# Performance work log

Measured on AMD Instinct MI355X. Metric: run time of the kernel, lower is better.

## Reference

```python
import jax, jax.numpy as jnp
import numpy as np

N_QUBITS = 4
N_LAYERS = 2
DIM = 1 << N_QUBITS  # 16-dim state vector

# --- fixed (parameter-free) CNOT entangler layers, precomputed as 16x16 permutations ---

def _cnot_perm(c, t):
    M = np.zeros((DIM, DIM), np.complex64)
    for b in range(DIM):
        b2 = b ^ (1 << (N_QUBITS - 1 - t)) if (b >> (N_QUBITS - 1 - c)) & 1 else b
        M[b2, b] = 1.0
    return M

def _entangler(r):
    E = np.eye(DIM, dtype=np.complex64)
    for i in range(N_QUBITS):  # pennylane applies CNOT(i, (i+r)%n) sequentially
        E = _cnot_perm(i, (i + r) % N_QUBITS) @ E
    return E

ENT = [jnp.asarray(_entangler((l % (N_QUBITS - 1)) + 1)) for l in range(N_LAYERS)]
# Z_TABLE[b, w] = <b| Z_w |b>
Z_TABLE = jnp.asarray(np.array([[1.0 - 2.0 * ((b >> (N_QUBITS - 1 - w)) & 1) for w in range(N_QUBITS)] for b in range(DIM)], np.float32))


def _rot(phi, theta, omega):
    # pennylane Rot = RZ(omega) @ RY(theta) @ RZ(phi)
    c = jnp.cos(theta / 2).astype(jnp.complex64)
    s = jnp.sin(theta / 2).astype(jnp.complex64)
    a = jnp.exp(-0.5j * (phi + omega)) * c
    b = -jnp.exp(0.5j * (phi - omega)) * s
    cc = jnp.exp(-0.5j * (phi - omega)) * s
    d = jnp.exp(0.5j * (phi + omega)) * c
    return jnp.stack([jnp.stack([a, b]), jnp.stack([cc, d])])


def _vqc_unitary(weights):
    # weights: [N_LAYERS, N_QUBITS, 3] -> 16x16 unitary for StronglyEntanglingLayers
    U = jnp.eye(DIM, dtype=jnp.complex64)
    for l in range(N_LAYERS):
        R = _rot(weights[l, 0, 0], weights[l, 0, 1], weights[l, 0, 2])
        for q in range(1, N_QUBITS):  # wire 0 is most-significant bit -> left kron factor
            R = jnp.kron(R, _rot(weights[l, q, 0], weights[l, q, 1], weights[l, q, 2]))
        U = ENT[l] @ (R @ U)
    return U


def _vqc(x, weights):
    # x: [..., 4] rotation angles; AngleEmbedding uses RX: RX(a)|0> = [cos(a/2), -i sin(a/2)]
    c = jnp.cos(x / 2).astype(jnp.complex64)
    s = jnp.sin(x / 2).astype(jnp.complex64)
    amp = jnp.stack([c, -1j * s], axis=-1)  # [..., 4, 2]
    psi0 = jnp.einsum('...a,...b,...c,...d->...abcd', amp[..., 0, :], amp[..., 1, :], amp[..., 2, :], amp[..., 3, :])
    psi0 = psi0.reshape(x.shape[:-1] + (DIM,))
    U = _vqc_unitary(weights)
    psi = jnp.einsum('ij,...j->...i', U, psi0)
    probs = psi.real ** 2 + psi.imag ** 2
    return probs @ Z_TABLE  # [..., 4] PauliZ expectation values


def setup_inputs() -> dict:
    key = jax.random.key(0)
    k0, k1, k2, k3 = jax.random.split(key, 4)
    H = 768
    B, S = 8, 2048
    embeddings = jax.random.normal(k0, (B, S, H), dtype=jnp.float32)
    lim = 1.0 / np.sqrt(H)
    Wq = jax.random.normal(k1, (N_QUBITS, H), dtype=jnp.float32) * lim
    Wk = jax.random.normal(k2, (N_QUBITS, H), dtype=jnp.float32) * lim
    bq = jnp.zeros((N_QUBITS,), jnp.float32)
    bk = jnp.zeros((N_QUBITS,), jnp.float32)
    vqc_weights = jax.random.uniform(k3, (N_LAYERS, N_QUBITS, 3), dtype=jnp.float32) * (2.0 * np.pi)
    return {'embeddings': embeddings, 'Wq': Wq, 'bq': bq, 'Wk': Wk, 'bk': bk, 'vqc_weights': vqc_weights}


def reference(embeddings, Wq, bq, Wk, bk, vqc_weights):
    Q = jnp.einsum('bsh,qh->bsq', embeddings, Wq) + bq  # [B,S,4]
    K = jnp.einsum('bsh,qh->bsq', embeddings, Wk) + bk
    Qv = _vqc(Q, vqc_weights)  # [B,S,4]
    Kv = _vqc(K, vqc_weights)
    attn = jax.nn.softmax(jnp.einsum('bsq,btq->bst', Qv, Kv), axis=-1)  # [B,S,S]
    return jnp.einsum('bst,bth->bsh', attn, embeddings)
```

## Files before the change

kernel.cpp:

```cpp
#include <hip/hip_runtime.h>

#define NB 8
#define NS 2048
#define NH 768
#define NPOS (NB*NS)

typedef short short8 __attribute__((ext_vector_type(8)));
typedef float floatx4 __attribute__((ext_vector_type(4)));

__device__ __forceinline__ unsigned pack_bf16(unsigned b0, unsigned b1) {
  return __builtin_amdgcn_perm(b1, b0, 0x07060302u);
}

#define GLOAD_LDS16(gp, lp) __builtin_amdgcn_global_load_lds( \
  (const __attribute__((address_space(1))) unsigned int*)(gp), \
  (__attribute__((address_space(3))) unsigned int*)(lp), 16, 0, 0)

__global__ __launch_bounds__(384) void epre_kernel(
    const float* __restrict__ E, const float* __restrict__ wts,
    float* __restrict__ Vre, float* __restrict__ Vim,
    unsigned short* __restrict__ ET) {
  int tc = blockIdx.x, hb = blockIdx.y, b = blockIdx.z;
  int tid = threadIdx.x;

  if (tc == 0 && hb == 0 && b == 0 && tid < 16) {
    int j = tid;
    float ar[16], ai[16];
#pragma unroll
    for (int i = 0; i < 16; i++) { ar[i] = (i == j) ? 1.f : 0.f; ai[i] = 0.f; }
#pragma unroll
    for (int l = 0; l < 2; l++) {
#pragma unroll
      for (int q = 0; q < 4; q++) {
        float phi = wts[(l*4+q)*3+0];
        float th  = wts[(l*4+q)*3+1];
        float om  = wts[(l*4+q)*3+2];
        float ct = cosf(0.5f*th), st = sinf(0.5f*th);
        float sm = 0.5f*(phi+om), df = 0.5f*(phi-om);
        float cs = cosf(sm), ss = sinf(sm), cd = cosf(df), sd = sinf(df);
        float Ar =  cs*ct, Ai = -ss*ct;
        float Br = -cd*st, Bi = -sd*st;
        float Cr =  cd*st, Ci = -sd*st;
        float Dr =  cs*ct, Di =  ss*ct;
        int pb = 1 << (3-q);
#pragma unroll
        for (int b0 = 0; b0 < 16; b0++) {
          if (b0 & pb) continue;
          int b1 = b0 | pb;
          float xr = ar[b0], xi = ai[b0], yr = ar[b1], yi = ai[b1];
          ar[b0] = Ar*xr - Ai*xi + Br*yr - Bi*yi;
          ai[b0] = Ar*xi + Ai*xr + Br*yi + Bi*yr;
          ar[b1] = Cr*xr - Ci*xi + Dr*yr - Di*yi;
          ai[b1] = Cr*xi + Ci*xr + Dr*yi + Di*yr;
        }
      }
      const int r = (l == 0) ? 1 : 2;
#pragma unroll
      for (int i2 = 0; i2 < 4; i2++) {
        int cb = 1 << (3-i2);
        int tb = 1 << (3-((i2+r)&3));
#pragma unroll
        for (int b0 = 0; b0 < 16; b0++) {
          if ((b0 & cb) && !(b0 & tb)) {
            int b1 = b0 | tb;
            float tr = ar[b0], ti = ai[b0];
            ar[b0] = ar[b1]; ai[b0] = ai[b1];
            ar[b1] = tr;     ai[b1] = ti;
          }
        }
      }
    }
    int pc = __popc((unsigned)j) & 3;
#pragma unroll
    for (int i = 0; i < 16; i++) {
      float vr = ar[i], vi = ai[i], orr, oi;
      if      (pc == 0) { orr =  vr; oi =  vi; }
      else if (pc == 1) { orr =  vi; oi = -vr; }
      else if (pc == 2) { orr = -vr; oi = -vi; }
      else              { orr = -vi; oi =  vr; }
      Vre[i*16+j] = orr;
      Vim[i*16+j] = oi;
    }
  }

  size_t tbase = ((size_t)((b*4 + hb)*64 + tc)) * 12288;
  const float* Eb = E + (size_t)b*NS*NH + (size_t)tc*32*NH + hb*192;
#pragma unroll
  for (int u = 0; u < 2; u++) {
    int unit = tid + 384*u;
    int q2 = unit / 192, h2 = unit % 192;
    unsigned hi4[4], lo4[4];
#pragma unroll
    for (int jp = 0; jp < 4; jp++) {
      float ea = Eb[(size_t)(q2*8 + 2*jp    )*NH + h2];
      float eb = Eb[(size_t)(q2*8 + 2*jp + 1)*NH + h2];
      unsigned ba = __float_as_uint(ea), bb = __float_as_uint(eb);
      float la = ea - __uint_as_float(ba & 0xFFFF0000u);
      float lb = eb - __uint_as_float(bb & 0xFFFF0000u);
      hi4[jp] = pack_bf16(ba, bb);
      lo4[jp] = pack_bf16(__float_as_uint(la), __float_as_uint(lb));
    }
    int off = h2*32 + ((q2 ^ ((h2>>1)&3))*8);
    *(uint4*)&ET[tbase + off]        = make_uint4(hi4[0],hi4[1],hi4[2],hi4[3]);
    *(uint4*)&ET[tbase + 6144 + off] = make_uint4(lo4[0],lo4[1],lo4[2],lo4[3]);
  }
}

__global__ __launch_bounds__(256) void proj_vqc_kernel(
    const float* __restrict__ E, const float* __restrict__ Wq, const float* __restrict__ bq,
    const float* __restrict__ Wk, const float* __restrict__ bk,
    const float* __restrict__ Vre, const float* __restrict__ Vim,
    float* __restrict__ Qv, float* __restrict__ Kv) {
  __shared__ __align__(16) float WqL[768*4];
  __shared__ __align__(16) float WkL[768*4];
  __shared__ float Vsh[2][16*17];
  int tid = threadIdx.x;
  for (int idx = tid; idx < 768*4; idx += 256) {
    int e = idx >> 2, w = idx & 3;
    WqL[e*4+w] = Wq[w*768+e];
    WkL[e*4+w] = Wk[w*768+e];
  }
  if (tid < 256) {
    int i = tid >> 4, jj = tid & 15;
    Vsh[0][i*17+jj] = Vre[tid];
    Vsh[1][i*17+jj] = Vim[tid];
  }
  __syncthreads();
  float bqr0=bq[0], bqr1=bq[1], bqr2=bq[2], bqr3=bq[3];
  float bkr0=bk[0], bkr1=bk[1], bkr2=bk[2], bkr3=bk[3];
  int lane = tid & 63;
  int wid  = blockIdx.x*4 + (tid >> 6);
  int nw   = gridDim.x*4;
  int grp  = lane >> 4;
  int i    = lane & 15;
  for (int pos = wid; pos < NPOS; pos += nw) {
    const float* er = E + (size_t)pos*768;
    float pq[4] = {0.f,0.f,0.f,0.f};
    float pk[4] = {0.f,0.f,0.f,0.f};
#pragma unroll
    for (int k2 = 0; k2 < 3; k2++) {
      float4 ev = *(const float4*)(er + lane*4 + 256*k2);
#pragma unroll
      for (int jj = 0; jj < 4; jj++) {
        int e = lane*4 + 256*k2 + jj;
        float evs = (jj==0) ? ev.x : (jj==1) ? ev.y : (jj==2) ? ev.z : ev.w;
        float4 wq4 = *(const float4*)&WqL[e*4];
        float4 wk4 = *(const float4*)&WkL[e*4];
        pq[0] += evs*wq4.x; pq[1] += evs*wq4.y; pq[2] += evs*wq4.z; pq[3] += evs*wq4.w;
        pk[0] += evs*wk4.x; pk[1] += evs*wk4.y; pk[2] += evs*wk4.z; pk[3] += evs*wk4.w;
      }
    }
    float part[8];
#pragma unroll
    for (int w = 0; w < 8; w++) {
      float v = (w < 4) ? pq[w] : pk[w-4];
      v += __shfl_xor(v, 32); v += __shfl_xor(v, 16); v += __shfl_xor(v, 8);
      v += __shfl_xor(v, 4);  v += __shfl_xor(v, 2);  v += __shfl_xor(v, 1);
      part[w] = v;
    }
    if (grp < 2) {
      float a0,a1,a2,a3;
      if (grp == 0) { a0=part[0]+bqr0; a1=part[1]+bqr1; a2=part[2]+bqr2; a3=part[3]+bqr3; }
      else          { a0=part[4]+bkr0; a1=part[5]+bkr1; a2=part[6]+bkr2; a3=part[7]+bkr3; }
      float c0=cosf(0.5f*a0), s0=sinf(0.5f*a0);
      float c1=cosf(0.5f*a1), s1=sinf(0.5f*a1);
      float c2=cosf(0.5f*a2), s2=sinf(0.5f*a2);
      float c3=cosf(0.5f*a3), s3=sinf(0.5f*a3);
      float m[16];
#pragma unroll
      for (int j2 = 0; j2 < 16; j2++) {
        float f0 = (j2 & 8) ? s0 : c0;
        float f1 = (j2 & 4) ? s1 : c1;
        float f2 = (j2 & 2) ? s2 : c2;
        float f3 = (j2 & 1) ? s3 : c3;
        m[j2] = f0*f1*f2*f3;
      }
      float re = 0.f, im = 0.f;
#pragma unroll
      for (int j2 = 0; j2 < 16; j2++) {
        re += Vsh[0][i*17+j2]*m[j2];
        im += Vsh[1][i*17+j2]*m[j2];
      }
      float pr = re*re + im*im;
      float r0 = (i & 8) ? -pr : pr;
      float r1 = (i & 4) ? -pr : pr;
      float r2 = (i & 2) ? -pr : pr;
      float r3 = (i & 1) ? -pr : pr;
#pragma unroll
      for (int off = 8; off >= 1; off >>= 1) {
        r0 += __shfl_xor(r0, off);
        r1 += __shfl_xor(r1, off);
        r2 += __shfl_xor(r2, off);
        r3 += __shfl_xor(r3, off);
      }
      if (i == 0) {
        float* dst = (grp == 0 ? Qv : Kv) + (size_t)pos*4;
        dst[0]=r0; dst[1]=r1; dst[2]=r2; dst[3]=r3;
      }
    }
  }
}

#define TKC 32

__global__ __launch_bounds__(512, 4) void attn_kernel(
    const unsigned short* __restrict__ ET, const float* __restrict__ Qv,
    const float* __restrict__ Kv, float* __restrict__ out) {
  int sblk = blockIdx.x;
  int hblk = blockIdx.y;
  int b    = blockIdx.z;
  int tid  = threadIdx.x;
  int lane = tid & 63;
  int w    = tid >> 6;

  __shared__ __align__(16) unsigned short sA[8192];
  __shared__ __align__(16) unsigned short sB[2][12288];
  __shared__ __align__(16) float kvf[2][TKC][4];
  __shared__ float denp[128*4];
  __shared__ float dfin[128];

  const unsigned short* tE = ET + ((size_t)((b*4 + hblk)*64)) * 12288;
  const float* Kvb = Kv + (size_t)b*NS*4;

  int sP = tid & 127, qP = tid >> 7;
  float4 qv = *(const float4*)&Qv[((size_t)(b*NS + sblk*128) + sP)*4];
  float den_acc = 0.f;

  int sh = w & 1, hh = w >> 1;
  floatx4 acc[4][3];
#pragma unroll
  for (int i = 0; i < 4; i++)
#pragma unroll
    for (int jt = 0; jt < 3; jt++) acc[i][jt] = floatx4{0.f,0.f,0.f,0.f};

  int m16 = lane & 15, q16 = lane >> 4;
  int cidx = (q16 ^ ((m16 >> 1) & 3)) * 8;
  int t16 = tid * 8;

  GLOAD_LDS16(tE + t16,        &sB[0][t16]);
  GLOAD_LDS16(tE + 4096 + t16, &sB[0][4096 + t16]);
  GLOAD_LDS16(tE + 8192 + t16, &sB[0][8192 + t16]);
  if (tid < 32) GLOAD_LDS16(Kvb + tid*4, &kvf[0][0][0] + tid*4);

  for (int tc = 0; tc < NS; tc += TKC) {
    int ci = tc >> 5;
    int cb = ci & 1;
    __syncthreads();

    {
      unsigned hi4[4], lo4[4];
      float dsum = 0.f;
#pragma unroll
      for (int jp = 0; jp < 4; jp++) {
        float4 ka = *(const float4*)&kvf[cb][qP*8 + 2*jp][0];
        float4 kb = *(const float4*)&kvf[cb][qP*8 + 2*jp + 1][0];
        float arga = qv.x*ka.x + qv.y*ka.y + qv.z*ka.z + qv.w*ka.w;
        float argb = qv.x*kb.x + qv.y*kb.y + qv.z*kb.z + qv.w*kb.w;
        float pa = __expf(arga), pb = __expf(argb);
        dsum += pa + pb;
        unsigned bpa = __float_as_uint(pa), bpb = __float_as_uint(pb);
        float lpa = pa - __uint_as_float(bpa & 0xFFFF0000u);
        float lpb = pb - __uint_as_float(bpb & 0xFFFF0000u);
        hi4[jp] = pack_bf16(bpa, bpb);
        lo4[jp] = pack_bf16(__float_as_uint(lpa), __float_as_uint(lpb));
      }
      den_acc += dsum;
      int offA = sP*32 + ((qP ^ ((sP>>1)&3))*8);
      *(uint4*)&sA[offA]        = make_uint4(hi4[0],hi4[1],hi4[2],hi4[3]);
      *(uint4*)&sA[4096 + offA] = make_uint4(lo4[0],lo4[1],lo4[2],lo4[3]);
    }

    __syncthreads();

    if (tc + TKC < NS) {
      const unsigned short* nE = tE + (size_t)(ci+1)*12288;
      int nb = cb ^ 1;
      GLOAD_LDS16(nE + t16,        &sB[nb][t16]);
      GLOAD_LDS16(nE + 4096 + t16, &sB[nb][4096 + t16]);
      GLOAD_LDS16(nE + 8192 + t16, &sB[nb][8192 + t16]);
      if (tid < 32) GLOAD_LDS16(Kvb + (size_t)(tc+TKC)*4 + tid*4, &kvf[nb][0][0] + tid*4);
    }

    short8 ah[4], al[4];
#pragma unroll
    for (int i = 0; i < 4; i++) {
      int srow = sh*64 + i*16 + m16;
      ah[i] = __builtin_bit_cast(short8, *(const uint4*)&sA[srow*TKC + cidx]);
      al[i] = __builtin_bit_cast(short8, *(const uint4*)&sA[4096 + srow*TKC + cidx]);
    }
#pragma unroll
    for (int jt = 0; jt < 3; jt++) {
      int hrow = hh*48 + jt*16 + m16;
      short8 bh_ = __builtin_bit_cast(short8, *(const uint4*)&sB[cb][hrow*TKC + cidx]);
      short8 bl_ = __builtin_bit_cast(short8, *(const uint4*)&sB[cb][6144 + hrow*TKC + cidx]);
#pragma unroll
      for (int i = 0; i < 4; i++) {
        acc[i][jt] = __builtin_amdgcn_mfma_f32_16x16x32_bf16(ah[i], bl_, acc[i][jt], 0, 0, 0);
        acc[i][jt] = __builtin_amdgcn_mfma_f32_16x16x32_bf16(al[i], bh_, acc[i][jt], 0, 0, 0);
        acc[i][jt] = __builtin_amdgcn_mfma_f32_16x16x32_bf16(ah[i], bh_, acc[i][jt], 0, 0, 0);
      }
    }
  }

  __syncthreads();
  denp[sP*4 + qP] = den_acc;
  __syncthreads();
  if (tid < 128) {
    dfin[tid] = denp[tid*4] + denp[tid*4+1] + denp[tid*4+2] + denp[tid*4+3];
  }
  __syncthreads();

  float* ob = out + ((size_t)(b*NS + sblk*128))*NH + hblk*192;
#pragma unroll
  for (int i = 0; i < 4; i++) {
#pragma unroll
    for (int reg = 0; reg < 4; reg++) {
      int row = q16*4 + reg;
      int s_loc = sh*64 + i*16 + row;
      float invd = 1.0f / dfin[s_loc];
#pragma unroll
      for (int jt = 0; jt < 3; jt++) {
        int h_loc = hh*48 + jt*16 + m16;
        ob[(size_t)s_loc*NH + h_loc] = acc[i][jt][reg] * invd;
      }
    }
  }
}

extern "C" void kernel_launch(void* const* d_in, const int* in_sizes, int n_in,
                              void* d_out, int out_size, void* d_ws, size_t ws_size,
                              hipStream_t stream) {
  const float* E   = (const float*)d_in[0];
  const float* Wq  = (const float*)d_in[1];
  const float* bq  = (const float*)d_in[2];
  const float* Wk  = (const float*)d_in[3];
  const float* bk  = (const float*)d_in[4];
  const float* wts = (const float*)d_in[5];
  float* ws  = (float*)d_ws;
  float* Vre = ws;
  float* Vim = ws + 256;
  float* Qv  = ws + 512;
  float* Kv  = Qv + (size_t)NPOS*4;
  unsigned short* ET = (unsigned short*)(Kv + (size_t)NPOS*4);
  float* out = (float*)d_out;

  epre_kernel<<<dim3(64, 4, 8), 384, 0, stream>>>(E, wts, Vre, Vim, ET);
  proj_vqc_kernel<<<1024, 256, 0, stream>>>(E, Wq, bq, Wk, bk, Vre, Vim, Qv, Kv);
  attn_kernel<<<dim3(16, 4, 8), 512, 0, stream>>>(ET, Qv, Kv, out);
}
```

Baseline: 281.9 us.

## Software-pipeline softmax probability computation one chunk ahead of MFMA

Restructures the attention main loop so each chunk's exp/bf16-split probabilities are computed in registers one iteration ahead, overlapping with the MFMA work on the previous chunk. Kv values are now loaded straight from global memory into registers instead of staged through an LDS buffer, which removes the kvf shared array. Each iteration only stores the precomputed probabilities to LDS between barriers. This raises register pressure (8 float4 Kv values plus the packed probabilities) under a 512-thread, 4-block launch bound, which could force spills or lower occupancy.

```diff
diff --git a/kernel.cpp b/kernel.cpp
--- a/kernel.cpp
+++ b/kernel.cpp
@@ -215,7 +215,6 @@
 
   __shared__ __align__(16) unsigned short sA[8192];
   __shared__ __align__(16) unsigned short sB[2][12288];
-  __shared__ __align__(16) float kvf[2][TKC][4];
   __shared__ float denp[128*4];
   __shared__ float dfin[128];
 
@@ -225,6 +224,7 @@
   int sP = tid & 127, qP = tid >> 7;
   float4 qv = *(const float4*)&Qv[((size_t)(b*NS + sblk*128) + sP)*4];
   float den_acc = 0.f;
+  int offA = sP*32 + ((qP ^ ((sP>>1)&3))*8);
 
   int sh = w & 1, hh = w >> 1;
   floatx4 acc[4][3];
@@ -237,50 +237,37 @@
   int cidx = (q16 ^ ((m16 >> 1) & 3)) * 8;
   int t16 = tid * 8;
 
-  GLOAD_LDS16(tE + t16,        &sB[0][t16]);
-  GLOAD_LDS16(tE + 4096 + t16, &sB[0][4096 + t16]);
-  GLOAD_LDS16(tE + 8192 + t16, &sB[0][8192 + t16]);
-  if (tid < 32) GLOAD_LDS16(Kvb + tid*4, &kvf[0][0][0] + tid*4);
-
-  for (int tc = 0; tc < NS; tc += TKC) {
-    int ci = tc >> 5;
-    int cb = ci & 1;
-    __syncthreads();
-
-    {
-      unsigned hi4[4], lo4[4];
-      float dsum = 0.f;
-#pragma unroll
-      for (int jp = 0; jp < 4; jp++) {
-        float4 ka = *(const float4*)&kvf[cb][qP*8 + 2*jp][0];
-        float4 kb = *(const float4*)&kvf[cb][qP*8 + 2*jp + 1][0];
-        float arga = qv.x*ka.x + qv.y*ka.y + qv.z*ka.z + qv.w*ka.w;
-        float argb = qv.x*kb.x + qv.y*kb.y + qv.z*kb.z + qv.w*kb.w;
-        float pa = __expf(arga), pb = __expf(argb);
-        dsum += pa + pb;
-        unsigned bpa = __float_as_uint(pa), bpb = __float_as_uint(pb);
-        float lpa = pa - __uint_as_float(bpa & 0xFFFF0000u);
-        float lpb = pb - __uint_as_float(bpb & 0xFFFF0000u);
-        hi4[jp] = pack_bf16(bpa, bpb);
-        lo4[jp] = pack_bf16(__float_as_uint(lpa), __float_as_uint(lpb));
-      }
-      den_acc += dsum;
-      int offA = sP*32 + ((qP ^ ((sP>>1)&3))*8);
-      *(uint4*)&sA[offA]        = make_uint4(hi4[0],hi4[1],hi4[2],hi4[3]);
-      *(uint4*)&sA[4096 + offA] = make_uint4(lo4[0],lo4[1],lo4[2],lo4[3]);
-    }
-
-    __syncthreads();
-
-    if (tc + TKC < NS) {
-      const unsigned short* nE = tE + (size_t)(ci+1)*12288;
-      int nb = cb ^ 1;
-      GLOAD_LDS16(nE + t16,        &sB[nb][t16]);
-      GLOAD_LDS16(nE + 4096 + t16, &sB[nb][4096 + t16]);
-      GLOAD_LDS16(nE + 8192 + t16, &sB[nb][8192 + t16]);
-      if (tid < 32) GLOAD_LDS16(Kvb + (size_t)(tc+TKC)*4 + tid*4, &kvf[nb][0][0] + tid*4);
-    }
-
+  uint4 ph, pl;
+
+  auto kvload = [&](int tb, float4* kvr) {
+    const float* kvp = Kvb + (size_t)(tb + qP*8)*4;
+#pragma unroll
+    for (int j = 0; j < 8; j++) kvr[j] = *(const float4*)(kvp + j*4);
+  };
+
+  auto pcompute = [&](const float4* kvr) {
+    unsigned hi4[4], lo4[4];
+    float dsum = 0.f;
+#pragma unroll
+    for (int jp = 0; jp < 4; jp++) {
+      float4 ka = kvr[2*jp];
+      float4 kb = kvr[2*jp+1];
+      float arga = qv.x*ka.x + qv.y*ka.y + qv.z*ka.z + qv.w*ka.w;
+      float argb = qv.x*kb.x + qv.y*kb.y + qv.z*kb.z + qv.w*kb.w;
+      float pa = __expf(arga), pb = __expf(argb);
+      dsum += pa + pb;
+      unsigned bpa = __float_as_uint(pa), bpb = __float_as_uint(pb);
+      float lpa = pa - __uint_as_float(bpa & 0xFFFF0000u);
+      float lpb = pb - __uint_as_float(bpb & 0xFFFF0000u);
+      hi4[jp] = pack_bf16(bpa, bpb);
+      lo4[jp] = pack_bf16(__float_as_uint(lpa), __float_as_uint(lpb));
+    }
+    den_acc += dsum;
+    ph = make_uint4(hi4[0],hi4[1],hi4[2],hi4[3]);
+    pl = make_uint4(lo4[0],lo4[1],lo4[2],lo4[3]);
+  };
+
+  auto do_mfma = [&](const unsigned short* sBc) {
     short8 ah[4], al[4];
 #pragma unroll
     for (int i = 0; i < 4; i++) {
@@ -291,8 +278,8 @@
 #pragma unroll
     for (int jt = 0; jt < 3; jt++) {
       int hrow = hh*48 + jt*16 + m16;
-      short8 bh_ = __builtin_bit_cast(short8, *(const uint4*)&sB[cb][hrow*TKC + cidx]);
-      short8 bl_ = __builtin_bit_cast(short8, *(const uint4*)&sB[cb][6144 + hrow*TKC + cidx]);
+      short8 bh_ = __builtin_bit_cast(short8, *(const uint4*)&sBc[hrow*TKC + cidx]);
+      short8 bl_ = __builtin_bit_cast(short8, *(const uint4*)&sBc[6144 + hrow*TKC + cidx]);
 #pragma unroll
       for (int i = 0; i < 4; i++) {
         acc[i][jt] = __builtin_amdgcn_mfma_f32_16x16x32_bf16(ah[i], bl_, acc[i][jt], 0, 0, 0);
@@ -300,9 +287,45 @@
         acc[i][jt] = __builtin_amdgcn_mfma_f32_16x16x32_bf16(ah[i], bh_, acc[i][jt], 0, 0, 0);
       }
     }
-  }
-
-  __syncthreads();
+  };
+
+  {
+    float4 kvr[8];
+    kvload(0, kvr);
+    GLOAD_LDS16(tE + t16,        &sB[0][0] + t16);
+    GLOAD_LDS16(tE + 4096 + t16, &sB[0][0] + 4096 + t16);
+    GLOAD_LDS16(tE + 8192 + t16, &sB[0][0] + 8192 + t16);
+    pcompute(kvr);
+  }
+
+  for (int ci = 0; ci < 63; ci++) {
+    int cb = ci & 1;
+
+    __syncthreads();
+    *(uint4*)&sA[offA]        = ph;
+    *(uint4*)&sA[4096 + offA] = pl;
+    __syncthreads();
+
+    float4 kvr[8];
+    kvload((ci+1)*TKC, kvr);
+
+    const unsigned short* nE = tE + (size_t)(ci+1)*12288;
+    unsigned short* sBn = &sB[cb^1][0];
+    GLOAD_LDS16(nE + t16,        sBn + t16);
+    GLOAD_LDS16(nE + 4096 + t16, sBn + 4096 + t16);
+    GLOAD_LDS16(nE + 8192 + t16, sBn + 8192 + t16);
+
+    pcompute(kvr);
+
+    do_mfma(&sB[cb][0]);
+  }
+
+  __syncthreads();
+  *(uint4*)&sA[offA]        = ph;
+  *(uint4*)&sA[4096 + offA] = pl;
+  __syncthreads();
+  do_mfma(&sB[1][0]);
+
   denp[sP*4 + qP] = den_acc;
   __syncthreads();
   if (tid < 128) {
```

Result: no change. 286.4 us (+1.6%).
